# Kernel tuning notes

Hardware: AMD Instinct MI355X
Metric: run time of the kernel (lower is better)

The kernel has to match this reference:

```python
import jax, jax.numpy as jnp
import numpy as np

N_NODES = 10000
N_EDGES = 640000
IN_C = 128
OUT_C = 128
BOND_F = 16


def setup_inputs() -> dict:
    key = jax.random.key(0)
    ks = jax.random.split(key, 8)
    x = jax.random.normal(ks[0], (N_NODES, IN_C), dtype=jnp.float32)
    edge_attr = jax.random.normal(ks[1], (N_EDGES, BOND_F), dtype=jnp.float32)
    edge_weight = jax.random.uniform(ks[2], (N_EDGES, 1), dtype=jnp.float32)
    W_bond = jax.random.normal(ks[3], (BOND_F, IN_C), dtype=jnp.float32) * 0.1
    b_bond = jax.random.normal(ks[4], (IN_C,), dtype=jnp.float32) * 0.1
    W_lin = jax.random.normal(ks[5], (IN_C, OUT_C), dtype=jnp.float32) * 0.05
    b_lin = jax.random.normal(ks[6], (OUT_C,), dtype=jnp.float32) * 0.05
    edge_index = jax.random.randint(ks[7], (2, N_EDGES), 0, N_NODES, dtype=jnp.int32)
    return {"x": x, "edge_attr": edge_attr, "edge_weight": edge_weight,
            "W_bond": W_bond, "b_bond": b_bond, "W_lin": W_lin, "b_lin": b_lin,
            "edge_index": edge_index}


def _inv_sqrt_deg(idx, n, dtype):
    # degree via segment_sum of ones; inf (deg==0) mapped to 0
    deg = jax.ops.segment_sum(jnp.ones_like(idx, dtype=dtype), idx, num_segments=n)
    return jnp.where(deg > 0, jax.lax.rsqrt(jnp.maximum(deg, 1.0)) * (deg > 0), 0.0).astype(dtype)


def reference(x, edge_attr, edge_weight, W_bond, b_bond, W_lin, b_lin, edge_index):
    n = x.shape[0]
    # bond encoder: Linear on edge features -> [E, C]
    edge_emb = edge_attr @ W_bond + b_bond
    # append self-loops with zero edge embedding and unit edge weight
    sl = jnp.arange(n, dtype=edge_index.dtype)
    ei = jnp.concatenate([edge_index, jnp.stack([sl, sl])], axis=1)  # [2, E+N]
    emb = jnp.concatenate([edge_emb, jnp.zeros((n, edge_emb.shape[1]), edge_emb.dtype)], axis=0)
    ew = jnp.concatenate([edge_weight, jnp.ones((n, 1), edge_weight.dtype)], axis=0)
    row, col = ei[0], ei[1]
    norm = _inv_sqrt_deg(row, n, x.dtype)[row] * _inv_sqrt_deg(col, n, x.dtype)[col]
    # gather + GELU(exact/erf) + degree norm + edge weight, then scatter-sum
    msg = jax.nn.gelu(x[row] + emb, approximate=False) * norm[:, None] * ew
    out = jax.ops.segment_sum(msg, col, num_segments=n)  # [N, C]
    return out @ W_lin + b_lin
```

## Files before the change

### kernel.cpp

```cpp
#include <hip/hip_runtime.h>
#include <hip/hip_bf16.h>
#include <math.h>

#define N_NODES 10000
#define N_EDGES 640000
#define C 128
#define BF 16
#define MAXD 160
#define PADS 4

typedef int iv4 __attribute__((ext_vector_type(4)));
typedef float fv4 __attribute__((ext_vector_type(4)));

__device__ __forceinline__ float2 bf2_to_f2(unsigned u) {
    union { unsigned x; float f; } lo, hi;
    lo.x = (u & 0xffffu) << 16;
    hi.x = u & 0xffff0000u;
    float2 r; r.x = lo.f; r.y = hi.f; return r;
}

__device__ __forceinline__ float fast_gelu(float z) {
    float z2 = z * z;
    float p  = z * fmaf(0.044715f, z2, 1.0f);
    float e  = __builtin_amdgcn_exp2f(-2.3022082f * p);
    float r  = __builtin_amdgcn_rcpf(1.0f + e);
    return z * r;
}

__global__ __launch_bounds__(256) void k_prep(
    const float* __restrict__ x, __hip_bfloat16* __restrict__ xb,
    const int* __restrict__ ei, const float* __restrict__ ew,
    int* __restrict__ dr, int* __restrict__ dc, iv4* __restrict__ bs)
{
    int b = blockIdx.x;
    if (b < 1250) {
        int i = (b * 256 + threadIdx.x) * 4;
        float4 v = *(const float4*)(x + i);
        xb[i + 0] = __float2bfloat16(v.x);
        xb[i + 1] = __float2bfloat16(v.y);
        xb[i + 2] = __float2bfloat16(v.z);
        xb[i + 3] = __float2bfloat16(v.w);
        return;
    }
    int e = (b - 1250) * 256 + threadIdx.x;
    int r = ei[e];
    int c = ei[N_EDGES + e];
    atomicAdd(&dr[r << PADS], 1);
    int pp = atomicAdd(&dc[c << PADS], 1);
    if (pp < MAXD) {
        iv4 v;
        v.x = e;
        v.y = r;
        v.z = __float_as_int(ew[e]);
        v.w = 0;
        bs[(size_t)c * MAXD + pp] = v;
    }
}

#define EDGE_COMPUTE(q0, q1, q2, q3, xf, s) do {                          \
    float m0 = bbv.x, m1 = bbv.y;                                         \
    m0 = fmaf(q0.x, wb[0].x, m0);   m1 = fmaf(q0.x, wb[0].y, m1);         \
    m0 = fmaf(q0.y, wb[1].x, m0);   m1 = fmaf(q0.y, wb[1].y, m1);         \
    m0 = fmaf(q0.z, wb[2].x, m0);   m1 = fmaf(q0.z, wb[2].y, m1);         \
    m0 = fmaf(q0.w, wb[3].x, m0);   m1 = fmaf(q0.w, wb[3].y, m1);         \
    m0 = fmaf(q1.x, wb[4].x, m0);   m1 = fmaf(q1.x, wb[4].y, m1);         \
    m0 = fmaf(q1.y, wb[5].x, m0);   m1 = fmaf(q1.y, wb[5].y, m1);         \
    m0 = fmaf(q1.z, wb[6].x, m0);   m1 = fmaf(q1.z, wb[6].y, m1);         \
    m0 = fmaf(q1.w, wb[7].x, m0);   m1 = fmaf(q1.w, wb[7].y, m1);         \
    m0 = fmaf(q2.x, wb[8].x, m0);   m1 = fmaf(q2.x, wb[8].y, m1);         \
    m0 = fmaf(q2.y, wb[9].x, m0);   m1 = fmaf(q2.y, wb[9].y, m1);         \
    m0 = fmaf(q2.z, wb[10].x, m0);  m1 = fmaf(q2.z, wb[10].y, m1);        \
    m0 = fmaf(q2.w, wb[11].x, m0);  m1 = fmaf(q2.w, wb[11].y, m1);        \
    m0 = fmaf(q3.x, wb[12].x, m0);  m1 = fmaf(q3.x, wb[12].y, m1);        \
    m0 = fmaf(q3.y, wb[13].x, m0);  m1 = fmaf(q3.y, wb[13].y, m1);        \
    m0 = fmaf(q3.z, wb[14].x, m0);  m1 = fmaf(q3.z, wb[14].y, m1);        \
    m0 = fmaf(q3.w, wb[15].x, m0);  m1 = fmaf(q3.w, wb[15].y, m1);        \
    a0 = fmaf(fast_gelu(xf.x + m0), (s), a0);                             \
    a1 = fmaf(fast_gelu(xf.y + m1), (s), a1);                             \
} while (0)

__global__ __launch_bounds__(512) void k_node(
    const __hip_bfloat16* __restrict__ xb, const float* __restrict__ ea,
    const float* __restrict__ Wb, const float* __restrict__ bb,
    const int* __restrict__ dr, const int* __restrict__ dc,
    const iv4* __restrict__ bs,
    const float* __restrict__ Wl, const float* __restrict__ bl,
    float* __restrict__ out)
{
    int n = blockIdx.x;
    int t = threadIdx.x;
    int w = t >> 6;
    int p = t & 63;

    __shared__ int   se[MAXD];
    __shared__ int   sr[MAXD];
    __shared__ float ss[MAXD];

    int cnt = dc[n << PADS]; if (cnt > MAXD) cnt = MAXD;

    if (t < cnt) {
        iv4 h = bs[(size_t)n * MAXD + t];
        se[t] = h.x;
        sr[t] = h.y;
        ss[t] = rsqrtf((float)(dr[h.y << PADS] + 1)) * __int_as_float(h.z);
    }

    float2 wb[BF];
#pragma unroll
    for (int k = 0; k < BF; k++)
        wb[k] = *(const float2*)(Wb + (size_t)k * C + 2 * p);
    float2 bbv = *(const float2*)(bb + 2 * p);
    __syncthreads();

    float a0 = 0.f, a1 = 0.f;
    const unsigned* xbu = (const unsigned*)xb;

    for (int j = w; j < cnt; j += 8) {
        int e = __builtin_amdgcn_readfirstlane(se[j]);
        int r = __builtin_amdgcn_readfirstlane(sr[j]);
        float s = ss[j];
        const fv4* ep = (const fv4*)ea + (size_t)e * 4;
        fv4 q0 = ep[0], q1 = ep[1], q2 = ep[2], q3 = ep[3];
        float2 xf = bf2_to_f2(xbu[(size_t)r * 64 + p]);
        EDGE_COMPUTE(q0, q1, q2, q3, xf, s);
    }

    __shared__ float2 shp[8][64];
    __shared__ __align__(16) float shs[C];
    __shared__ float sho[4][C];

    shp[w][p] = make_float2(a0, a1);
    __syncthreads();
    if (t < 64) {
        float vx = 0.f, vy = 0.f;
#pragma unroll
        for (int k = 0; k < 8; k++) { vx += shp[k][t].x; vy += shp[k][t].y; }
        float icn = rsqrtf((float)(dc[n << PADS] + 1));
        float irn = rsqrtf((float)(dr[n << PADS] + 1));
        float2 xf = bf2_to_f2(xbu[(size_t)n * 64 + t]);
        shs[2 * t]     = (vx + fast_gelu(xf.x) * irn) * icn;
        shs[2 * t + 1] = (vy + fast_gelu(xf.y) * irn) * icn;
    }
    __syncthreads();

    int ch = t & (C - 1), q = t >> 7;
    float o = 0.f;
    const float4* shv = (const float4*)shs + q * 8;
    const float* wcol = Wl + (size_t)(q * 32) * C + ch;
#pragma unroll
    for (int k4 = 0; k4 < 8; k4++) {
        float4 sv = shv[k4];
        o = fmaf(sv.x, wcol[(size_t)(k4 * 4 + 0) * C], o);
        o = fmaf(sv.y, wcol[(size_t)(k4 * 4 + 1) * C], o);
        o = fmaf(sv.z, wcol[(size_t)(k4 * 4 + 2) * C], o);
        o = fmaf(sv.w, wcol[(size_t)(k4 * 4 + 3) * C], o);
    }
    sho[q][ch] = o;
    __syncthreads();
    if (t < C) out[(size_t)n * C + t] = bl[t] + sho[0][t] + sho[1][t] + sho[2][t] + sho[3][t];
}

__global__ void k_deg(const int* __restrict__ ei, int* __restrict__ dr, int* __restrict__ dc) {
    int e = blockIdx.x * blockDim.x + threadIdx.x;
    if (e < N_EDGES) {
        atomicAdd(&dr[ei[e]], 1);
        atomicAdd(&dc[ei[N_EDGES + e]], 1);
    }
}

__global__ __launch_bounds__(1024) void k_scan_fb(
    const int* __restrict__ dr, const int* __restrict__ dc,
    int* __restrict__ off, float* __restrict__ ir, float* __restrict__ ic)
{
    __shared__ int shp[1024];
    int t = threadIdx.x;
    int base = t * 10;
    int loc[10];
    int s = 0;
#pragma unroll
    for (int j = 0; j < 10; j++) {
        int i = base + j;
        int v = (i < N_NODES) ? dc[i] : 0;
        loc[j] = s;
        s += v;
    }
    shp[t] = s;
    __syncthreads();
    for (int st = 1; st < 1024; st <<= 1) {
        int a = (t >= st) ? shp[t - st] : 0;
        __syncthreads();
        shp[t] += a;
        __syncthreads();
    }
    int excl = shp[t] - s;
#pragma unroll
    for (int j = 0; j < 10; j++) {
        int i = base + j;
        if (i < N_NODES) {
            off[i] = excl + loc[j];
            ir[i] = rsqrtf((float)(dr[i] + 1));
            ic[i] = rsqrtf((float)(dc[i] + 1));
        }
    }
    if (t == 1023) off[N_NODES] = shp[1023];
}

__global__ void k_scatter(const int* __restrict__ ei, const int* __restrict__ off,
                          int* __restrict__ cur, int* __restrict__ bucket) {
    int e = blockIdx.x * blockDim.x + threadIdx.x;
    if (e < N_EDGES) {
        int c = ei[N_EDGES + e];
        int pos = atomicAdd(&cur[c], 1);
        bucket[off[c] + pos] = e;
    }
}

__global__ __launch_bounds__(512) void k_node_fb(
    const float* __restrict__ x,
    const float* __restrict__ ea, const float* __restrict__ ew,
    const float* __restrict__ Wb, const float* __restrict__ bb,
    const int* __restrict__ ei,
    const float* __restrict__ ir, const float* __restrict__ ic,
    const int* __restrict__ off, const int* __restrict__ bucket,
    const float* __restrict__ Wl, const float* __restrict__ bl,
    float* __restrict__ out)
{
    int n = blockIdx.x;
    int t = threadIdx.x & (C - 1);
    int g = threadIdx.x >> 7;
    float icn = ic[n];
    float wb[BF];
#pragma unroll
    for (int k = 0; k < BF; k++) wb[k] = Wb[(size_t)k * C + t];
    float bbt = bb[t];
    float acc = 0.0f;
    if (g == 0) acc = fast_gelu(x[(size_t)n * C + t]) * (ir[n] * icn);
    int o0 = off[n], o1 = off[n + 1];
    for (int i = o0 + g; i < o1; i += 4) {
        int e = __builtin_amdgcn_readfirstlane(bucket[i]);
        int r = ei[e];
        float s = ir[r] * icn * ew[e];
        const float4* eapt = (const float4*)(ea + (size_t)e * BF);
        float4 q0 = eapt[0], q1 = eapt[1], q2 = eapt[2], q3 = eapt[3];
        float emb = bbt;
        emb = fmaf(q0.x, wb[0], emb);  emb = fmaf(q0.y, wb[1], emb);
        emb = fmaf(q0.z, wb[2], emb);  emb = fmaf(q0.w, wb[3], emb);
        emb = fmaf(q1.x, wb[4], emb);  emb = fmaf(q1.y, wb[5], emb);
        emb = fmaf(q1.z, wb[6], emb);  emb = fmaf(q1.w, wb[7], emb);
        emb = fmaf(q2.x, wb[8], emb);  emb = fmaf(q2.y, wb[9], emb);
        emb = fmaf(q2.z, wb[10], emb); emb = fmaf(q2.w, wb[11], emb);
        emb = fmaf(q3.x, wb[12], emb); emb = fmaf(q3.y, wb[13], emb);
        emb = fmaf(q3.z, wb[14], emb); emb = fmaf(q3.w, wb[15], emb);
        acc = fmaf(fast_gelu(x[(size_t)r * C + t] + emb), s, acc);
    }
    __shared__ float shp[4][C];
    __shared__ float shs[C];
    shp[g][t] = acc;
    __syncthreads();
    if (threadIdx.x < C) {
        int k = threadIdx.x;
        shs[k] = shp[0][k] + shp[1][k] + shp[2][k] + shp[3][k];
    }
    __syncthreads();
    float o = 0.0f;
    int k0 = g * 32;
#pragma unroll 8
    for (int j = 0; j < 32; j++) {
        int k = k0 + j;
        o = fmaf(shs[k], Wl[(size_t)k * C + t], o);
    }
    shp[g][t] = o;
    __syncthreads();
    if (threadIdx.x < C) {
        int c = threadIdx.x;
        out[(size_t)n * C + c] = bl[c] + shp[0][c] + shp[1][c] + shp[2][c] + shp[3][c];
    }
}

extern "C" void kernel_launch(void* const* d_in, const int* in_sizes, int n_in,
                              void* d_out, int out_size, void* d_ws, size_t ws_size,
                              hipStream_t stream) {
    const float* x  = (const float*)d_in[0];
    const float* ea = (const float*)d_in[1];
    const float* ew = (const float*)d_in[2];
    const float* Wb = (const float*)d_in[3];
    const float* bb = (const float*)d_in[4];
    const float* Wl = (const float*)d_in[5];
    const float* bl = (const float*)d_in[6];
    const int*   ei = (const int*)d_in[7];
    float* out = (float*)d_out;

    const int PADN = 10240 << PADS;
    const size_t need_full = (size_t)N_NODES * MAXD * 16
                           + (size_t)640000 * 4 + (size_t)2 * PADN * 4;

    if (ws_size >= need_full) {
        iv4* bs = (iv4*)d_ws;
        unsigned* xbu = (unsigned*)(bs + (size_t)N_NODES * MAXD);
        int* dr = (int*)(xbu + 640000);
        int* dc = dr + PADN;
        __hip_bfloat16* xb = (__hip_bfloat16*)xbu;

        (void)hipMemsetAsync(dr, 0, 2 * (size_t)PADN * sizeof(int), stream);
        k_prep<<<3750, 256, 0, stream>>>(x, xb, ei, ew, dr, dc, bs);
        k_node<<<N_NODES, 512, 0, stream>>>(
            xb, ea, Wb, bb, dr, dc, bs, Wl, bl, out);
    } else {
        int* bucket = (int*)d_ws;
        int* off = bucket + 640000;
        int* dr  = off + 10304;
        int* dc  = dr + 10240;
        int* cur = dc + 10240;
        float* ir = (float*)(cur + 10240);
        float* ic = ir + 10240;

        (void)hipMemsetAsync(dr, 0, 3 * 10240 * sizeof(int), stream);
        k_deg<<<(N_EDGES + 255) / 256, 256, 0, stream>>>(ei, dr, dc);
        k_scan_fb<<<1, 1024, 0, stream>>>(dr, dc, off, ir, ic);
        k_scatter<<<(N_EDGES + 255) / 256, 256, 0, stream>>>(ei, off, cur, bucket);
        k_node_fb<<<N_NODES, 512, 0, stream>>>(
            x, ea, ew, Wb, bb, ei, ir, ic, off, bucket, Wl, bl, out);
    }
}
```

Before: 254.8 us.

## Process two destination nodes per block, sharing Wl loads and shared memory

Each 512-thread block now handles two destination nodes, with four waves per node for edge accumulation instead of eight. The final linear projection loads each Wl element once and applies it to both nodes, and shared memory is packed into one reused buffer. The aim is to halve the block count and amortise per-block setup (Wb loads, syncs, Wl reads). In exchange each node's edges are spread over fewer waves, so high-degree nodes take longer and load imbalance between the two nodes in a block can leave waves idle.

```diff
diff --git a/kernel.cpp b/kernel.cpp
--- a/kernel.cpp
+++ b/kernel.cpp
@@ -87,22 +87,32 @@
     const float* __restrict__ Wl, const float* __restrict__ bl,
     float* __restrict__ out)
 {
-    int n = blockIdx.x;
+    int n0 = blockIdx.x * 2;
     int t = threadIdx.x;
     int w = t >> 6;
     int p = t & 63;
-
-    __shared__ int   se[MAXD];
-    __shared__ int   sr[MAXD];
-    __shared__ float ss[MAXD];
-
-    int cnt = dc[n << PADS]; if (cnt > MAXD) cnt = MAXD;
-
-    if (t < cnt) {
-        iv4 h = bs[(size_t)n * MAXD + t];
-        se[t] = h.x;
-        sr[t] = h.y;
-        ss[t] = rsqrtf((float)(dr[h.y << PADS] + 1)) * __int_as_float(h.z);
+    int m = w >> 2;
+    int w4 = w & 3;
+
+    __shared__ __align__(16) char smbuf[8192];
+    int*   se = (int*)smbuf;
+    int*   sr = (int*)(smbuf + 1280);
+    float* ss = (float*)(smbuf + 2560);
+    float2* shp = (float2*)(smbuf + 4096);
+
+    int cnt0 = dc[n0 << PADS];       if (cnt0 > MAXD) cnt0 = MAXD;
+    int cnt1 = dc[(n0 + 1) << PADS]; if (cnt1 > MAXD) cnt1 = MAXD;
+
+    if (t < 2 * MAXD) {
+        int nn = (t >= MAXD) ? 1 : 0;
+        int sl = t - nn * MAXD;
+        int cc = nn ? cnt1 : cnt0;
+        if (sl < cc) {
+            iv4 h = bs[(size_t)(n0 + nn) * MAXD + sl];
+            se[t] = h.x;
+            sr[t] = h.y;
+            ss[t] = rsqrtf((float)(dr[h.y << PADS] + 1)) * __int_as_float(h.z);
+        }
     }
 
     float2 wb[BF];
@@ -114,50 +124,69 @@
 
     float a0 = 0.f, a1 = 0.f;
     const unsigned* xbu = (const unsigned*)xb;
-
-    for (int j = w; j < cnt; j += 8) {
-        int e = __builtin_amdgcn_readfirstlane(se[j]);
-        int r = __builtin_amdgcn_readfirstlane(sr[j]);
-        float s = ss[j];
+    int cnt  = m ? cnt1 : cnt0;
+    int base = m * MAXD;
+
+    for (int j = w4; j < cnt; j += 4) {
+        int e = __builtin_amdgcn_readfirstlane(se[base + j]);
+        int r = __builtin_amdgcn_readfirstlane(sr[base + j]);
+        float s = ss[base + j];
         const fv4* ep = (const fv4*)ea + (size_t)e * 4;
         fv4 q0 = ep[0], q1 = ep[1], q2 = ep[2], q3 = ep[3];
         float2 xf = bf2_to_f2(xbu[(size_t)r * 64 + p]);
         EDGE_COMPUTE(q0, q1, q2, q3, xf, s);
     }
 
-    __shared__ float2 shp[8][64];
-    __shared__ __align__(16) float shs[C];
-    __shared__ float sho[4][C];
-
-    shp[w][p] = make_float2(a0, a1);
-    __syncthreads();
-    if (t < 64) {
+    shp[w * 64 + p] = make_float2(a0, a1);
+    __syncthreads();
+
+    float* shs = (float*)smbuf;
+    if (t < 128) {
+        int mm = t >> 6, tt = t & 63;
         float vx = 0.f, vy = 0.f;
 #pragma unroll
-        for (int k = 0; k < 8; k++) { vx += shp[k][t].x; vy += shp[k][t].y; }
-        float icn = rsqrtf((float)(dc[n << PADS] + 1));
-        float irn = rsqrtf((float)(dr[n << PADS] + 1));
-        float2 xf = bf2_to_f2(xbu[(size_t)n * 64 + t]);
-        shs[2 * t]     = (vx + fast_gelu(xf.x) * irn) * icn;
-        shs[2 * t + 1] = (vy + fast_gelu(xf.y) * irn) * icn;
-    }
-    __syncthreads();
-
+        for (int k = 0; k < 4; k++) {
+            float2 v = shp[(mm * 4 + k) * 64 + tt];
+            vx += v.x; vy += v.y;
+        }
+        int nn = n0 + mm;
+        float icn = rsqrtf((float)(dc[nn << PADS] + 1));
+        float irn = rsqrtf((float)(dr[nn << PADS] + 1));
+        float2 xf = bf2_to_f2(xbu[(size_t)nn * 64 + tt]);
+        shs[mm * C + 2 * tt]     = (vx + fast_gelu(xf.x) * irn) * icn;
+        shs[mm * C + 2 * tt + 1] = (vy + fast_gelu(xf.y) * irn) * icn;
+    }
+    __syncthreads();
+
+    float* sho = (float*)(smbuf + 4096);
     int ch = t & (C - 1), q = t >> 7;
-    float o = 0.f;
-    const float4* shv = (const float4*)shs + q * 8;
+    float o0 = 0.f, o1 = 0.f;
+    const float4* sv0 = (const float4*)shs + q * 8;
+    const float4* sv1 = (const float4*)(shs + C) + q * 8;
     const float* wcol = Wl + (size_t)(q * 32) * C + ch;
 #pragma unroll
     for (int k4 = 0; k4 < 8; k4++) {
-        float4 sv = shv[k4];
-        o = fmaf(sv.x, wcol[(size_t)(k4 * 4 + 0) * C], o);
-        o = fmaf(sv.y, wcol[(size_t)(k4 * 4 + 1) * C], o);
-        o = fmaf(sv.z, wcol[(size_t)(k4 * 4 + 2) * C], o);
-        o = fmaf(sv.w, wcol[(size_t)(k4 * 4 + 3) * C], o);
-    }
-    sho[q][ch] = o;
-    __syncthreads();
-    if (t < C) out[(size_t)n * C + t] = bl[t] + sho[0][t] + sho[1][t] + sho[2][t] + sho[3][t];
+        float4 s0 = sv0[k4];
+        float4 s1 = sv1[k4];
+        float wl0 = wcol[(size_t)(k4 * 4 + 0) * C];
+        float wl1 = wcol[(size_t)(k4 * 4 + 1) * C];
+        float wl2 = wcol[(size_t)(k4 * 4 + 2) * C];
+        float wl3 = wcol[(size_t)(k4 * 4 + 3) * C];
+        o0 = fmaf(s0.x, wl0, o0);  o1 = fmaf(s1.x, wl0, o1);
+        o0 = fmaf(s0.y, wl1, o0);  o1 = fmaf(s1.y, wl1, o1);
+        o0 = fmaf(s0.z, wl2, o0);  o1 = fmaf(s1.z, wl2, o1);
+        o0 = fmaf(s0.w, wl3, o0);  o1 = fmaf(s1.w, wl3, o1);
+    }
+    sho[(q * 2 + 0) * C + ch] = o0;
+    sho[(q * 2 + 1) * C + ch] = o1;
+    __syncthreads();
+
+    if (t < 2 * C) {
+        int mm = t >> 7, c2 = t & (C - 1);
+        out[(size_t)(n0 + mm) * C + c2] = bl[c2]
+            + sho[(0 * 2 + mm) * C + c2] + sho[(1 * 2 + mm) * C + c2]
+            + sho[(2 * 2 + mm) * C + c2] + sho[(3 * 2 + mm) * C + c2];
+    }
 }
 
 __global__ void k_deg(const int* __restrict__ ei, int* __restrict__ dr, int* __restrict__ dc) {
@@ -303,7 +332,7 @@
 
         (void)hipMemsetAsync(dr, 0, 2 * (size_t)PADN * sizeof(int), stream);
         k_prep<<<3750, 256, 0, stream>>>(x, xb, ei, ew, dr, dc, bs);
-        k_node<<<N_NODES, 512, 0, stream>>>(
+        k_node<<<N_NODES / 2, 512, 0, stream>>>(
             xb, ea, Wb, bb, dr, dc, bs, Wl, bl, out);
     } else {
         int* bucket = (int*)d_ws;
```

Result: faster. 235.0 us (median of 2 runs) (-7.8%).
